# Kernel optimization log

Measured on AMD Instinct MI355X. Metric: run time of the kernel, lower is better.

The kernel has to match this reference:

```python
import jax, jax.numpy as jnp
import numpy as np

B, NA, NMAX, NC = 32, 8400, 32, 80
TOPK, ALPHA, BETA, EPS, BG_IDX = 13, 1.0, 6.0, 1e-9, 80
IMG = 640.0


def _ciou(box1, box2, eps=1e-7):
    # box1: (b, nmax, 1, 4) xyxy, box2: (b, 1, na, 4) xyxy -> CIoU (b, nmax, na)
    b1_x1, b1_y1, b1_x2, b1_y2 = (box1[..., 0], box1[..., 1], box1[..., 2], box1[..., 3])
    b2_x1, b2_y1, b2_x2, b2_y2 = (box2[..., 0], box2[..., 1], box2[..., 2], box2[..., 3])
    inter = (jnp.minimum(b1_x2, b2_x2) - jnp.maximum(b1_x1, b2_x1)).clip(0) * \
            (jnp.minimum(b1_y2, b2_y2) - jnp.maximum(b1_y1, b2_y1)).clip(0)
    w1, h1 = b1_x2 - b1_x1, b1_y2 - b1_y1 + eps
    w2, h2 = b2_x2 - b2_x1, b2_y2 - b2_y1 + eps
    union = w1 * h1 + w2 * h2 - inter + eps
    iou = inter / union
    cw = jnp.maximum(b1_x2, b2_x2) - jnp.minimum(b1_x1, b2_x1)
    ch = jnp.maximum(b1_y2, b2_y2) - jnp.minimum(b1_y1, b2_y1)
    c2 = cw * cw + ch * ch + eps
    rho2 = ((b2_x1 + b2_x2 - b1_x1 - b1_x2) ** 2 + (b2_y1 + b2_y2 - b1_y1 - b1_y2) ** 2) / 4.0
    v = (4.0 / np.pi ** 2) * (jnp.arctan(w2 / h2) - jnp.arctan(w1 / h1)) ** 2
    alpha = jax.lax.stop_gradient(v / (v - iou + (1.0 + eps)))
    return iou - (rho2 / c2 + v * alpha)


def _rand_boxes(key, shape):
    # well-formed xyxy boxes inside a 640x640 image
    k1, k2 = jax.random.split(key)
    xy = jax.random.uniform(k1, shape[:-1] + (2,), jnp.float32) * (IMG - 64.0)
    wh = jax.random.uniform(k2, shape[:-1] + (2,), jnp.float32) * 56.0 + 8.0
    return jnp.concatenate([xy, xy + wh], axis=-1)


def setup_inputs() -> dict:
    key = jax.random.key(0)
    ks = jax.random.split(key, 6)
    pd_scores = jax.random.uniform(ks[0], (B, NA, NC), jnp.float32)
    pd_bboxes = _rand_boxes(ks[1], (B, NA, 4))
    anc_points = jax.random.uniform(ks[2], (NA, 2), jnp.float32) * IMG
    gt_labels = jax.random.randint(ks[3], (B, NMAX, 1), 0, NC, dtype=jnp.int32)
    gt_bboxes = _rand_boxes(ks[4], (B, NMAX, 4))
    mask_gt = jnp.ones((B, NMAX, 1), jnp.float32)
    return {"pd_scores": pd_scores, "pd_bboxes": pd_bboxes, "anc_points": anc_points,
            "gt_labels": gt_labels, "gt_bboxes": gt_bboxes, "mask_gt": mask_gt}


def reference(pd_scores, pd_bboxes, anc_points, gt_labels, gt_bboxes, mask_gt):
    b, na, nc = pd_scores.shape
    nmax = gt_bboxes.shape[1]
    # pairwise CIoU between every GT and every predicted box: (b, nmax, na)
    overlaps = _ciou(gt_bboxes[:, :, None, :], pd_bboxes[:, None, :, :])
    # gather predicted class score at each GT's label: (b, nmax, na)
    p = jnp.transpose(pd_scores, (0, 2, 1))                     # (b, nc, na)
    scores = jnp.take_along_axis(p, gt_labels.astype(jnp.int32), axis=1)
    align_metric = (scores ** ALPHA) * (overlaps ** BETA)
    # top-k anchors per GT along the anchor axis, scatter to a boolean mask
    _, topk_idx = jax.lax.top_k(align_metric, TOPK)             # (b, nmax, topk)
    bi = jnp.arange(b)[:, None, None]
    gi = jnp.arange(nmax)[None, :, None]
    mask_pos = jnp.zeros((b, nmax, na), bool).at[bi, gi, topk_idx].set(True)
    target_gt_idx = jnp.argmax(mask_pos, axis=1)                # (b, na)
    fg_mask = mask_pos.sum(axis=1) > 0                          # (b, na)
    # gather assigned GT label / box per anchor
    target_labels = jnp.take_along_axis(gt_labels[..., 0].astype(jnp.int32), target_gt_idx, axis=1)
    target_bboxes = jnp.take_along_axis(gt_bboxes, target_gt_idx[..., None], axis=1)  # (b, na, 4)
    target_scores = jax.nn.one_hot(target_labels, nc, dtype=jnp.float32) * fg_mask[..., None]
    target_labels = jnp.where(fg_mask, target_labels, BG_IDX)
    # normalize target scores by mean positive overlap per anchor, clamped to [0, 1]
    mpf = mask_pos.astype(overlaps.dtype)
    pos_overlaps = jnp.clip((overlaps * mpf).sum(axis=1) / (mpf.sum(axis=1) + EPS), 0.0, 1.0)
    target_scores = target_scores * pos_overlaps[..., None]
    return target_labels, target_bboxes, target_scores, fg_mask, target_gt_idx
```

## Files before the change

kernel.cpp:

```cpp
#include <hip/hip_runtime.h>
#include <math.h>

#define BATCH 32
#define NA 8400
#define NMAX 32
#define NC 80
#define TOPK 13
#define THREADS 256
#define NPT 33
#define TILE 128
#define SSTRIDE 81

#define OFF_BOX 268800
#define OFF_SCR 1344000
#define OFF_FG  22848000
#define OFF_TGT 23116800

typedef float f32x4 __attribute__((ext_vector_type(4)));

__device__ __forceinline__ float ciou_f(float gx1, float gy1, float gx2, float gy2,
                                        float px1, float py1, float px2, float py2) {
    const float eps = 1e-7f;
    float iw = fmaxf(fminf(gx2, px2) - fmaxf(gx1, px1), 0.0f);
    float ih = fmaxf(fminf(gy2, py2) - fmaxf(gy1, py1), 0.0f);
    float inter = iw * ih;
    float w1 = gx2 - gx1, h1 = gy2 - gy1 + eps;
    float w2 = px2 - px1, h2 = py2 - py1 + eps;
    float uni = w1 * h1 + w2 * h2 - inter + eps;
    float iou = inter / uni;
    float cw = fmaxf(gx2, px2) - fminf(gx1, px1);
    float ch = fmaxf(gy2, py2) - fminf(gy1, py1);
    float c2 = cw * cw + ch * ch + eps;
    float dx = px1 + px2 - gx1 - gx2;
    float dy = py1 + py2 - gy1 - gy2;
    float rho2 = (dx * dx + dy * dy) / 4.0f;
    float dd = atanf(w2 / h2) - atanf(w1 / h1);
    float v = (float)(4.0 / (M_PI * M_PI)) * dd * dd;
    float alpha = v / (v - iou + (1.0f + eps));
    return iou - (rho2 / c2 + v * alpha);
}

__global__ __launch_bounds__(THREADS, 2) void metric_kernel(
    const float* __restrict__ pd_scores, const float* __restrict__ pd_bboxes,
    const int* __restrict__ gt_labels, const float* __restrict__ gt_bboxes,
    float* __restrict__ met, unsigned int* __restrict__ mask) {
    const int b = blockIdx.y;
    const int abase = blockIdx.x * TILE;
    const int tid = threadIdx.x;
    const int na_tile = min(TILE, NA - abase);
    const float eps = 1e-7f;

    if (tid < na_tile) mask[(size_t)b * NA + abase + tid] = 0u;

    __shared__ float ssc[TILE][SSTRIDE];
    __shared__ float4 spbox[TILE];
    __shared__ float sgx1[NMAX], sgy1[NMAX], sgx2[NMAX], sgy2[NMAX];
    __shared__ float sa1[NMAX], sat1[NMAX];
    __shared__ int   slbl[NMAX];

    if (tid < NMAX) {
        float4 g = ((const float4*)gt_bboxes)[b * NMAX + tid];
        float w1 = g.z - g.x, h1 = g.w - g.y + eps;
        sgx1[tid] = g.x; sgy1[tid] = g.y; sgx2[tid] = g.z; sgy2[tid] = g.w;
        sa1[tid]  = w1 * h1;
        sat1[tid] = atanf(w1 / h1);
        slbl[tid] = gt_labels[b * NMAX + tid];
    } else if (tid >= 128) {
        int al = tid - 128;
        if (al < na_tile)
            spbox[al] = ((const float4*)pd_bboxes)[(size_t)b * NA + abase + al];
    }

    const float4* srec4 = (const float4*)(pd_scores + ((size_t)b * NA + abase) * NC);
    const int nf4 = na_tile * 20;
    float4 r[10];
#pragma unroll
    for (int i = 0; i < 10; i++) {
        int f = tid + i * THREADS;
        if (f < nf4) r[i] = srec4[f];
    }
#pragma unroll
    for (int i = 0; i < 10; i++) {
        int f = tid + i * THREADS;
        if (f < nf4) {
            int a = f / 20, c = f % 20;
            float* d = &ssc[a][c * 4];
            d[0] = r[i].x; d[1] = r[i].y; d[2] = r[i].z; d[3] = r[i].w;
        }
    }
    __syncthreads();

    const int al = tid & (TILE - 1);
    const int gbase = (tid >> 7) * 16;
    if (al >= na_tile) return;

    float4 p = spbox[al];
    float w2 = p.z - p.x, h2 = p.w - p.y + eps;
    float a2  = w2 * h2;
    float at2 = atanf(w2 / h2);
    const size_t abs_a = (size_t)abase + al;

#pragma unroll
    for (int k = 0; k < 16; k++) {
        int gi = gbase + k;
        float gx1 = sgx1[gi], gy1 = sgy1[gi], gx2 = sgx2[gi], gy2 = sgy2[gi];
        float iw = fmaxf(fminf(gx2, p.z) - fmaxf(gx1, p.x), 0.0f);
        float ih = fmaxf(fminf(gy2, p.w) - fmaxf(gy1, p.y), 0.0f);
        float inter = iw * ih;
        float uni = sa1[gi] + a2 - inter + eps;
        float iou = inter / uni;
        float cw = fmaxf(gx2, p.z) - fminf(gx1, p.x);
        float ch = fmaxf(gy2, p.w) - fminf(gy1, p.y);
        float c2 = cw * cw + ch * ch + eps;
        float dx = p.x + p.z - gx1 - gx2;
        float dy = p.y + p.w - gy1 - gy2;
        float rho2 = (dx * dx + dy * dy) / 4.0f;
        float dd = at2 - sat1[gi];
        float v = (float)(4.0 / (M_PI * M_PI)) * dd * dd;
        float alpha = v / (v - iou + (1.0f + eps));
        float ov = iou - (rho2 / c2 + v * alpha);
        float sc = ssc[al][slbl[gi]];
        float ov2 = ov * ov;
        met[((size_t)b * NMAX + gi) * NA + abs_a] = sc * (ov2 * ov2 * ov2);
    }
}

__global__ __launch_bounds__(THREADS) void topk_kernel(
    const float* __restrict__ met, unsigned int* __restrict__ mask) {
    const int tid  = threadIdx.x;
    const int lane = tid & 63;
    const int w    = tid >> 6;
    const int bid  = blockIdx.x;
    const int b  = bid >> 5;
    const int gi = bid & 31;
    const float* mrow = met + ((size_t)b * NMAX + gi) * NA;

    float m[NPT];
#pragma unroll
    for (int j = 0; j < NPT; j++) {
        int a = j * THREADS + tid;
        m[j] = (a < NA) ? mrow[a] : -INFINITY;
    }

    float bv0 = -INFINITY, bv1 = -INFINITY;
    int   ba0 = 0x7FFFFFFF, ba1 = 0x7FFFFFFF;
#pragma unroll
    for (int j = 0; j < NPT; j++) {
        float v = m[j]; int a = j * THREADS + tid;
        bool beats0 = (v > bv0) || (v == bv0 && a < ba0);
        bool beats1 = (v > bv1) || (v == bv1 && a < ba1);
        if (beats0) { bv1 = bv0; ba1 = ba0; bv0 = v; ba0 = a; }
        else if (beats1) { bv1 = v; ba1 = a; }
    }
    bool valid1 = true;

    float rv = -INFINITY; int ra = 0x7FFFFFFF;
    for (int k = 0; k < TOPK; k++) {
        float v = bv0; int a = ba0;
#pragma unroll
        for (int s = 1; s < 64; s <<= 1) {
            float ov = __shfl_xor(v, s);
            int   oa = __shfl_xor(a, s);
            if (ov > v || (ov == v && oa < a)) { v = ov; a = oa; }
        }
        if (lane == k) { rv = v; ra = a; }
        if (ba0 == a) {
            if (valid1) { bv0 = bv1; ba0 = ba1; valid1 = false; }
            else {
                float nv = -INFINITY; int na_ = 0x7FFFFFFF;
#pragma unroll
                for (int j = 0; j < NPT; j++) {
                    float mv = m[j]; int ma = j * THREADS + tid;
                    bool below = (mv < v) || (mv == v && ma > a);
                    bool beats = (mv > nv) || (mv == nv && ma < na_);
                    if (below && beats) { nv = mv; na_ = ma; }
                }
                bv0 = nv; ba0 = na_;
            }
        }
    }

    __shared__ float lv[4 * TOPK];
    __shared__ int   la[4 * TOPK];
    if (lane < TOPK) { lv[w * TOPK + lane] = rv; la[w * TOPK + lane] = ra; }
    __syncthreads();

    if (w == 0) {
        float v = (lane < 4 * TOPK) ? lv[lane] : -INFINITY;
        int   a = (lane < 4 * TOPK) ? la[lane] : 0x7FFFFFFF;
        for (int k = 0; k < TOPK; k++) {
            float wv = v; int wa = a;
#pragma unroll
            for (int s = 1; s < 64; s <<= 1) {
                float ov = __shfl_xor(wv, s);
                int   oa = __shfl_xor(wa, s);
                if (ov > wv || (ov == wv && oa < wa)) { wv = ov; wa = oa; }
            }
            if (lane == 0) atomicOr(&mask[(size_t)b * NA + wa], 1u << gi);
            if (a == wa) { v = -INFINITY; a = 0x7FFFFFFF; }
        }
    }
}

__global__ __launch_bounds__(THREADS) void assign_score_kernel(
    const float* __restrict__ pd_bboxes, const int* __restrict__ gt_labels,
    const float* __restrict__ gt_bboxes, const unsigned int* __restrict__ mask,
    float* __restrict__ out) {
    const int tid = threadIdx.x;
    const int ab = blockIdx.x * THREADS;
    const int idx = ab + tid;
    __shared__ float spo[THREADS];
    __shared__ int   slb[THREADS];

    {
        int b = idx / NA;
        unsigned msk = mask[idx];
        int tgt = msk ? (__ffs(msk) - 1) : 0;
        float4 gb = ((const float4*)gt_bboxes)[b * NMAX + tgt];
        int lbl = gt_labels[b * NMAX + tgt];
        float4 p = ((const float4*)pd_bboxes)[idx];

        float sum = 0.0f;
        int cnt = 0;
        unsigned mm = msk;
        while (mm) {
            int i = __ffs(mm) - 1;
            mm &= mm - 1;
            float4 g = ((const float4*)gt_bboxes)[b * NMAX + i];
            sum += ciou_f(g.x, g.y, g.z, g.w, p.x, p.y, p.z, p.w);
            cnt++;
        }
        float po = fminf(fmaxf(sum / ((float)cnt + 1e-9f), 0.0f), 1.0f);

        bool fg = (msk != 0);
        __builtin_nontemporal_store(fg ? (float)lbl : 80.0f, &out[idx]);
        f32x4 gbv = { gb.x, gb.y, gb.z, gb.w };
        __builtin_nontemporal_store(gbv, (f32x4*)(out + OFF_BOX) + idx);
        __builtin_nontemporal_store(fg ? 1.0f : 0.0f, &out[OFF_FG + idx]);
        __builtin_nontemporal_store((float)tgt, &out[OFF_TGT + idx]);
        spo[tid] = po;
        slb[tid] = fg ? lbl : -1;
    }
    __syncthreads();

    f32x4* obase = (f32x4*)(out + OFF_SCR + (size_t)ab * NC);
#pragma unroll
    for (int i = 0; i < 20; i++) {
        int f = tid + i * THREADS;
        int a = f / 20, c = f % 20;
        int lbl = slb[a];
        f32x4 z = { 0.f, 0.f, 0.f, 0.f };
        if ((lbl >> 2) == c) z[lbl & 3] = spo[a];
        __builtin_nontemporal_store(z, obase + f);
    }
}

extern "C" void kernel_launch(void* const* d_in, const int* in_sizes, int n_in,
                              void* d_out, int out_size, void* d_ws, size_t ws_size,
                              hipStream_t stream) {
    const float* pd_scores = (const float*)d_in[0];
    const float* pd_bboxes = (const float*)d_in[1];
    const int*   gt_labels = (const int*)d_in[3];
    const float* gt_bboxes = (const float*)d_in[4];

    float* out = (float*)d_out;
    unsigned int* mask = (unsigned int*)d_ws;
    float* met = out + OFF_SCR;

    dim3 g1((NA + TILE - 1) / TILE, BATCH);
    metric_kernel<<<g1, THREADS, 0, stream>>>(pd_scores, pd_bboxes,
                                              gt_labels, gt_bboxes, met, mask);
    topk_kernel<<<BATCH * NMAX, THREADS, 0, stream>>>(met, mask);
    assign_score_kernel<<<BATCH * NA / THREADS, THREADS, 0, stream>>>(
        pd_bboxes, gt_labels, gt_bboxes, mask, out);
}
```

Baseline: 91.81 us.

## Fuse metric computation with per-segment top-k and add merge kernel

Replaces the separate metric and top-k kernels with a fused kernel in which each block covers a 576-anchor segment for one batch. It computes the align metric in 64-anchor chunks, prefetching the next chunk of scores in registers, and keeps a per-lane top-2 per GT. This yields per-segment top-13 candidates, and a small merge kernel reduces these to the final mask. The aim is to avoid writing and re-reading the full 32x8400 metric array per batch. The cost is a small grid (16x32 blocks) and recomputing CIoU from global memory whenever a lane's top-2 runs out.

```diff
diff --git a/kernel.cpp b/kernel.cpp
--- a/kernel.cpp
+++ b/kernel.cpp
@@ -7,9 +7,9 @@
 #define NC 80
 #define TOPK 13
 #define THREADS 256
-#define NPT 33
-#define TILE 128
-#define SSTRIDE 81
+#define NSEG 16
+#define SCH 9
+#define SEGA 576
 
 #define OFF_BOX 268800
 #define OFF_SCR 1344000
@@ -40,20 +40,22 @@
     return iou - (rho2 / c2 + v * alpha);
 }
 
-__global__ __launch_bounds__(THREADS, 2) void metric_kernel(
+__global__ __launch_bounds__(THREADS) void fused_topk_kernel(
     const float* __restrict__ pd_scores, const float* __restrict__ pd_bboxes,
     const int* __restrict__ gt_labels, const float* __restrict__ gt_bboxes,
-    float* __restrict__ met, unsigned int* __restrict__ mask) {
-    const int b = blockIdx.y;
-    const int abase = blockIdx.x * TILE;
-    const int tid = threadIdx.x;
-    const int na_tile = min(TILE, NA - abase);
+    float* __restrict__ pv, int* __restrict__ pi, unsigned int* __restrict__ mask) {
+    const int seg = blockIdx.x, b = blockIdx.y;
+    const int tid = threadIdx.x, lane = tid & 63, w = tid >> 6;
+    const int a0 = seg * SEGA;
     const float eps = 1e-7f;
 
-    if (tid < na_tile) mask[(size_t)b * NA + abase + tid] = 0u;
-
-    __shared__ float ssc[TILE][SSTRIDE];
-    __shared__ float4 spbox[TILE];
+    for (int i = tid; i < SEGA; i += THREADS) {
+        int a = a0 + i;
+        if (a < NA) mask[(size_t)b * NA + a] = 0u;
+    }
+
+    __shared__ float ssc[64][81];
+    __shared__ float4 spbox[64];
     __shared__ float sgx1[NMAX], sgy1[NMAX], sgx2[NMAX], sgy2[NMAX];
     __shared__ float sa1[NMAX], sat1[NMAX];
     __shared__ int   slbl[NMAX];
@@ -65,140 +67,188 @@
         sa1[tid]  = w1 * h1;
         sat1[tid] = atanf(w1 / h1);
         slbl[tid] = gt_labels[b * NMAX + tid];
-    } else if (tid >= 128) {
-        int al = tid - 128;
-        if (al < na_tile)
-            spbox[al] = ((const float4*)pd_bboxes)[(size_t)b * NA + abase + al];
-    }
-
-    const float4* srec4 = (const float4*)(pd_scores + ((size_t)b * NA + abase) * NC);
-    const int nf4 = na_tile * 20;
-    float4 r[10];
-#pragma unroll
-    for (int i = 0; i < 10; i++) {
-        int f = tid + i * THREADS;
-        if (f < nf4) r[i] = srec4[f];
-    }
-#pragma unroll
-    for (int i = 0; i < 10; i++) {
-        int f = tid + i * THREADS;
-        if (f < nf4) {
-            int a = f / 20, c = f % 20;
-            float* d = &ssc[a][c * 4];
-            d[0] = r[i].x; d[1] = r[i].y; d[2] = r[i].z; d[3] = r[i].w;
-        }
     }
     __syncthreads();
 
-    const int al = tid & (TILE - 1);
-    const int gbase = (tid >> 7) * 16;
-    if (al >= na_tile) return;
-
-    float4 p = spbox[al];
-    float w2 = p.z - p.x, h2 = p.w - p.y + eps;
-    float a2  = w2 * h2;
-    float at2 = atanf(w2 / h2);
-    const size_t abs_a = (size_t)abase + al;
-
-#pragma unroll
-    for (int k = 0; k < 16; k++) {
-        int gi = gbase + k;
-        float gx1 = sgx1[gi], gy1 = sgy1[gi], gx2 = sgx2[gi], gy2 = sgy2[gi];
-        float iw = fmaxf(fminf(gx2, p.z) - fmaxf(gx1, p.x), 0.0f);
-        float ih = fmaxf(fminf(gy2, p.w) - fmaxf(gy1, p.y), 0.0f);
-        float inter = iw * ih;
-        float uni = sa1[gi] + a2 - inter + eps;
-        float iou = inter / uni;
-        float cw = fmaxf(gx2, p.z) - fminf(gx1, p.x);
-        float ch = fmaxf(gy2, p.w) - fminf(gy1, p.y);
-        float c2 = cw * cw + ch * ch + eps;
-        float dx = p.x + p.z - gx1 - gx2;
-        float dy = p.y + p.w - gy1 - gy2;
-        float rho2 = (dx * dx + dy * dy) / 4.0f;
-        float dd = at2 - sat1[gi];
-        float v = (float)(4.0 / (M_PI * M_PI)) * dd * dd;
-        float alpha = v / (v - iou + (1.0f + eps));
-        float ov = iou - (rho2 / c2 + v * alpha);
-        float sc = ssc[al][slbl[gi]];
-        float ov2 = ov * ov;
-        met[((size_t)b * NMAX + gi) * NA + abs_a] = sc * (ov2 * ov2 * ov2);
-    }
-}
-
-__global__ __launch_bounds__(THREADS) void topk_kernel(
-    const float* __restrict__ met, unsigned int* __restrict__ mask) {
-    const int tid  = threadIdx.x;
-    const int lane = tid & 63;
-    const int w    = tid >> 6;
-    const int bid  = blockIdx.x;
-    const int b  = bid >> 5;
-    const int gi = bid & 31;
-    const float* mrow = met + ((size_t)b * NMAX + gi) * NA;
-
-    float m[NPT];
-#pragma unroll
-    for (int j = 0; j < NPT; j++) {
-        int a = j * THREADS + tid;
-        m[j] = (a < NA) ? mrow[a] : -INFINITY;
-    }
-
-    float bv0 = -INFINITY, bv1 = -INFINITY;
-    int   ba0 = 0x7FFFFFFF, ba1 = 0x7FFFFFFF;
-#pragma unroll
-    for (int j = 0; j < NPT; j++) {
-        float v = m[j]; int a = j * THREADS + tid;
-        bool beats0 = (v > bv0) || (v == bv0 && a < ba0);
-        bool beats1 = (v > bv1) || (v == bv1 && a < ba1);
-        if (beats0) { bv1 = bv0; ba1 = ba0; bv0 = v; ba0 = a; }
-        else if (beats1) { bv1 = v; ba1 = a; }
-    }
-    bool valid1 = true;
-
-    float rv = -INFINITY; int ra = 0x7FFFFFFF;
-    for (int k = 0; k < TOPK; k++) {
-        float v = bv0; int a = ba0;
+    const int nch = (a0 < NA) ? min(SCH, (NA - a0 + 63) / 64) : 0;
+
+    float tv0[8], tv1[8]; int ta0[8], ta1[8];
+#pragma unroll
+    for (int g = 0; g < 8; g++) {
+        tv0[g] = -INFINITY; tv1[g] = -INFINITY;
+        ta0[g] = 0x7FFFFFFF; ta1[g] = 0x7FFFFFFF;
+    }
+
+    float4 r[5]; float4 rbox;
+    if (nch > 0) {
+        int na_c = min(64, NA - a0);
+        int nf4 = na_c * 20;
+        const float4* s4 = (const float4*)(pd_scores + ((size_t)b * NA + a0) * NC);
+#pragma unroll
+        for (int i = 0; i < 5; i++) { int f = tid + i * THREADS; if (f < nf4) r[i] = s4[f]; }
+        if (tid < na_c) rbox = ((const float4*)pd_bboxes)[(size_t)b * NA + a0 + tid];
+    }
+
+    for (int c = 0; c < nch; ++c) {
+        const int abase = a0 + c * 64;
+        const int na_c = min(64, NA - abase);
+        const int nf4 = na_c * 20;
+        __syncthreads();
+#pragma unroll
+        for (int i = 0; i < 5; i++) {
+            int f = tid + i * THREADS;
+            if (f < nf4) {
+                int a = f / 20, cc = f % 20;
+                float* d = &ssc[a][cc * 4];
+                d[0] = r[i].x; d[1] = r[i].y; d[2] = r[i].z; d[3] = r[i].w;
+            }
+        }
+        if (tid < na_c) spbox[tid] = rbox;
+        __syncthreads();
+        if (c + 1 < nch) {
+            int ab2 = a0 + (c + 1) * 64;
+            int na2 = min(64, NA - ab2);
+            int nf2 = na2 * 20;
+            const float4* s4 = (const float4*)(pd_scores + ((size_t)b * NA + ab2) * NC);
+#pragma unroll
+            for (int i = 0; i < 5; i++) { int f = tid + i * THREADS; if (f < nf2) r[i] = s4[f]; }
+            if (tid < na2) rbox = ((const float4*)pd_bboxes)[(size_t)b * NA + ab2 + tid];
+        }
+        const bool av = (lane < na_c);
+        float4 p = spbox[lane];
+        float w2 = p.z - p.x, h2 = p.w - p.y + eps;
+        float a2  = w2 * h2;
+        float at2 = atanf(w2 / h2);
+        const int ga = abase + lane;
+#pragma unroll
+        for (int g = 0; g < 8; g++) {
+            int gi = (w << 3) + g;
+            float gx1 = sgx1[gi], gy1 = sgy1[gi], gx2 = sgx2[gi], gy2 = sgy2[gi];
+            float iw = fmaxf(fminf(gx2, p.z) - fmaxf(gx1, p.x), 0.0f);
+            float ih = fmaxf(fminf(gy2, p.w) - fmaxf(gy1, p.y), 0.0f);
+            float inter = iw * ih;
+            float uni = sa1[gi] + a2 - inter + eps;
+            float iou = inter / uni;
+            float cw = fmaxf(gx2, p.z) - fminf(gx1, p.x);
+            float ch = fmaxf(gy2, p.w) - fminf(gy1, p.y);
+            float c2 = cw * cw + ch * ch + eps;
+            float dx = p.x + p.z - gx1 - gx2;
+            float dy = p.y + p.w - gy1 - gy2;
+            float rho2 = (dx * dx + dy * dy) / 4.0f;
+            float dd = at2 - sat1[gi];
+            float v = (float)(4.0 / (M_PI * M_PI)) * dd * dd;
+            float alpha = v / (v - iou + (1.0f + eps));
+            float ov = iou - (rho2 / c2 + v * alpha);
+            float sc = ssc[lane][slbl[gi]];
+            float ov2 = ov * ov;
+            float metv = sc * (ov2 * ov2 * ov2);
+            float metf = av ? metv : -INFINITY;
+            int   ai   = av ? ga : 0x7FFFFFFF;
+            bool beats0 = (metf > tv0[g]) || (metf == tv0[g] && ai < ta0[g]);
+            bool beats1 = (metf > tv1[g]) || (metf == tv1[g] && ai < ta1[g]);
+            if (beats0) { tv1[g] = tv0[g]; ta1[g] = ta0[g]; tv0[g] = metf; ta0[g] = ai; }
+            else if (beats1) { tv1[g] = metf; ta1[g] = ai; }
+        }
+    }
+
+#pragma unroll
+    for (int g = 0; g < 8; g++) {
+        const int gi = (w << 3) + g;
+        float v0 = tv0[g], v1 = tv1[g];
+        int  aa0 = ta0[g], aa1 = ta1[g];
+        bool used1 = false;
+        float outv = -INFINITY; int outa = 0x7FFFFFFF;
+#pragma unroll 1
+        for (int k = 0; k < TOPK; ++k) {
+            float v = v0; int a = aa0;
+#pragma unroll
+            for (int s = 1; s < 64; s <<= 1) {
+                float ov = __shfl_xor(v, s);
+                int   oa = __shfl_xor(a, s);
+                if (ov > v || (ov == v && oa < a)) { v = ov; a = oa; }
+            }
+            if (lane == k) { outv = v; outa = a; }
+            if (aa0 == a) {
+                if (!used1) { v0 = v1; aa0 = aa1; used1 = true; }
+                else {
+                    float nv = -INFINITY; int na_ = 0x7FFFFFFF;
+                    int lbl = slbl[gi];
+                    float gx1 = sgx1[gi], gy1 = sgy1[gi], gx2 = sgx2[gi], gy2 = sgy2[gi];
+#pragma unroll 1
+                    for (int c2 = 0; c2 < SCH; ++c2) {
+                        int a2i = a0 + c2 * 64 + lane;
+                        if (a2i < NA) {
+                            float4 p = ((const float4*)pd_bboxes)[(size_t)b * NA + a2i];
+                            float w2 = p.z - p.x, h2 = p.w - p.y + eps;
+                            float a2  = w2 * h2;
+                            float at2 = atanf(w2 / h2);
+                            float iw = fmaxf(fminf(gx2, p.z) - fmaxf(gx1, p.x), 0.0f);
+                            float ih = fmaxf(fminf(gy2, p.w) - fmaxf(gy1, p.y), 0.0f);
+                            float inter = iw * ih;
+                            float uni = sa1[gi] + a2 - inter + eps;
+                            float iou = inter / uni;
+                            float cw = fmaxf(gx2, p.z) - fminf(gx1, p.x);
+                            float ch = fmaxf(gy2, p.w) - fminf(gy1, p.y);
+                            float c2v = cw * cw + ch * ch + eps;
+                            float dx = p.x + p.z - gx1 - gx2;
+                            float dy = p.y + p.w - gy1 - gy2;
+                            float rho2 = (dx * dx + dy * dy) / 4.0f;
+                            float dd = at2 - sat1[gi];
+                            float vv = (float)(4.0 / (M_PI * M_PI)) * dd * dd;
+                            float alpha = vv / (vv - iou + (1.0f + eps));
+                            float ovl = iou - (rho2 / c2v + vv * alpha);
+                            float sc = pd_scores[((size_t)b * NA + a2i) * NC + lbl];
+                            float ov2 = ovl * ovl;
+                            float mv = sc * (ov2 * ov2 * ov2);
+                            bool below = (mv < v) || (mv == v && a2i > a);
+                            bool beats = (mv > nv) || (mv == nv && a2i < na_);
+                            if (below && beats) { nv = mv; na_ = a2i; }
+                        }
+                    }
+                    v0 = nv; aa0 = na_;
+                }
+            }
+        }
+        if (lane < TOPK) {
+            size_t base = (((size_t)b * NMAX + gi) * NSEG + seg) * TOPK + lane;
+            pv[base] = outv; pi[base] = outa;
+        }
+    }
+}
+
+__global__ __launch_bounds__(THREADS) void merge_kernel(
+    const float* __restrict__ pv, const int* __restrict__ pi,
+    unsigned int* __restrict__ mask) {
+    const int row = blockIdx.x * 4 + (threadIdx.x >> 6);
+    const int lane = threadIdx.x & 63;
+    const int b = row >> 5, gi = row & 31;
+    const float* rv = pv + (size_t)row * NSEG * TOPK;
+    const int*   ri = pi + (size_t)row * NSEG * TOPK;
+
+    float cv[4]; int ci_[4];
+#pragma unroll
+    for (int j = 0; j < 4; j++) {
+        int s = lane + j * 64;
+        if (s < NSEG * TOPK) { cv[j] = rv[s]; ci_[j] = ri[s]; }
+        else { cv[j] = -INFINITY; ci_[j] = 0x7FFFFFFF; }
+    }
+#pragma unroll 1
+    for (int k = 0; k < TOPK; ++k) {
+        float bv = cv[0]; int ba = ci_[0];
+#pragma unroll
+        for (int j = 1; j < 4; j++)
+            if (cv[j] > bv || (cv[j] == bv && ci_[j] < ba)) { bv = cv[j]; ba = ci_[j]; }
+        float v = bv; int a = ba;
 #pragma unroll
         for (int s = 1; s < 64; s <<= 1) {
             float ov = __shfl_xor(v, s);
             int   oa = __shfl_xor(a, s);
             if (ov > v || (ov == v && oa < a)) { v = ov; a = oa; }
         }
-        if (lane == k) { rv = v; ra = a; }
-        if (ba0 == a) {
-            if (valid1) { bv0 = bv1; ba0 = ba1; valid1 = false; }
-            else {
-                float nv = -INFINITY; int na_ = 0x7FFFFFFF;
-#pragma unroll
-                for (int j = 0; j < NPT; j++) {
-                    float mv = m[j]; int ma = j * THREADS + tid;
-                    bool below = (mv < v) || (mv == v && ma > a);
-                    bool beats = (mv > nv) || (mv == nv && ma < na_);
-                    if (below && beats) { nv = mv; na_ = ma; }
-                }
-                bv0 = nv; ba0 = na_;
-            }
-        }
-    }
-
-    __shared__ float lv[4 * TOPK];
-    __shared__ int   la[4 * TOPK];
-    if (lane < TOPK) { lv[w * TOPK + lane] = rv; la[w * TOPK + lane] = ra; }
-    __syncthreads();
-
-    if (w == 0) {
-        float v = (lane < 4 * TOPK) ? lv[lane] : -INFINITY;
-        int   a = (lane < 4 * TOPK) ? la[lane] : 0x7FFFFFFF;
-        for (int k = 0; k < TOPK; k++) {
-            float wv = v; int wa = a;
-#pragma unroll
-            for (int s = 1; s < 64; s <<= 1) {
-                float ov = __shfl_xor(wv, s);
-                int   oa = __shfl_xor(wa, s);
-                if (ov > wv || (ov == wv && oa < wa)) { wv = ov; wa = oa; }
-            }
-            if (lane == 0) atomicOr(&mask[(size_t)b * NA + wa], 1u << gi);
-            if (a == wa) { v = -INFINITY; a = 0x7FFFFFFF; }
-        }
+        if (lane == k) atomicOr(&mask[(size_t)b * NA + a], 1u << gi);
+#pragma unroll
+        for (int j = 0; j < 4; j++)
+            if (ci_[j] == a) { cv[j] = -INFINITY; ci_[j] = 0x7FFFFFFF; }
     }
 }
 
@@ -265,12 +315,13 @@
 
     float* out = (float*)d_out;
     unsigned int* mask = (unsigned int*)d_ws;
-    float* met = out + OFF_SCR;
-
-    dim3 g1((NA + TILE - 1) / TILE, BATCH);
-    metric_kernel<<<g1, THREADS, 0, stream>>>(pd_scores, pd_bboxes,
-                                              gt_labels, gt_bboxes, met, mask);
-    topk_kernel<<<BATCH * NMAX, THREADS, 0, stream>>>(met, mask);
+    float* pv = out + OFF_SCR;
+    int*   pi = (int*)(out + OFF_SCR + BATCH * NMAX * NSEG * TOPK);
+
+    dim3 gf(NSEG, BATCH);
+    fused_topk_kernel<<<gf, THREADS, 0, stream>>>(pd_scores, pd_bboxes,
+                                                  gt_labels, gt_bboxes, pv, pi, mask);
+    merge_kernel<<<BATCH * NMAX / 4, THREADS, 0, stream>>>(pv, pi, mask);
     assign_score_kernel<<<BATCH * NA / THREADS, THREADS, 0, stream>>>(
         pd_bboxes, gt_labels, gt_bboxes, mask, out);
 }
```

Result: slower. 212.1 us (+131.0%).
